# Optimization experiments

Hardware: AMD Instinct MI355X
Metric: run time of the kernel (lower is better)

The kernel has to match this reference:

```python
import jax, jax.numpy as jnp
import numpy as np
import math

N_NODES, N_EDGES = 10000, 160000
CS, CZ, CH, NH, PQ, PV = 384, 128, 192, 12, 4, 8
INF, EPS = 100000.0, 1e-8


def setup_inputs() -> dict:
    key = jax.random.key(0)
    ks = iter(jax.random.split(key, 48))

    def rn(shape, scale=1.0):
        return jax.random.normal(next(ks), shape, jnp.float32) * scale

    def lin(din, dout):
        return rn((din, dout), 1.0 / math.sqrt(din)), jnp.zeros((dout,), jnp.float32)

    s = rn((N_NODES, CS))
    z = rn((N_EDGES, CZ))
    edge_index = jax.random.randint(next(ks), (2, N_EDGES), 0, N_NODES)
    # proper random rotations via QR (sign-corrected)
    A = rn((N_NODES, 3, 3))
    Q, R = jnp.linalg.qr(A)
    rots = Q * jnp.sign(jnp.diagonal(R, axis1=-2, axis2=-1))[:, None, :]
    trans = rn((N_NODES, 3), 10.0)
    mask = jnp.ones((N_NODES,), jnp.float32)
    Ww1, bw1 = lin(2 * CS + CZ, CH)
    Ww2, bw2 = lin(CH, CH)
    Ww3, bw3 = lin(CH, NH)
    Wv1, bv1 = lin(CS + CZ, CH)
    Wv2, bv2 = lin(CH, CH)
    Wv3, bv3 = lin(CH, CH)
    Wq, bq = lin(CS, NH * PQ * 3)
    Wkv, bkv = lin(CS, NH * (PQ + PV) * 3)
    Wb, bb = lin(CZ, NH)
    Wdz, bdz = lin(CZ, CZ // 4)
    Wo, bo = lin(NH * (CZ // 4 + CH // NH + PV * 4), CS)
    hw = jnp.full((NH,), math.log(math.e - 1.0), jnp.float32)  # softplus^-1(1)
    return dict(s=s, z=z, edge_index=edge_index, rots=rots, trans=trans, mask=mask,
                Ww1=Ww1, bw1=bw1, Ww2=Ww2, bw2=bw2, Ww3=Ww3, bw3=bw3,
                Wv1=Wv1, bv1=bv1, Wv2=Wv2, bv2=bv2, Wv3=Wv3, bv3=bv3,
                Wq=Wq, bq=bq, Wkv=Wkv, bkv=bkv, Wb=Wb, bb=bb,
                Wdz=Wdz, bdz=bdz, Wo=Wo, bo=bo, hw=hw)


def _points(flat, rots, t, P):
    # flat [N, 3P] is coord-major (split into 3 chunks then stacked last): p[n, p, c] = flat[n, c*P + p]
    p = flat.reshape(flat.shape[0], 3, P).transpose(0, 2, 1)
    return jnp.einsum('nij,npj->npi', rots, p) + t[:, None, :]


def _forward(s, z, edge_index, rots, trans, mask,
             Ww1, bw1, Ww2, bw2, Ww3, bw3,
             Wv1, bv1, Wv2, bv2, Wv3, bv3,
             Wq, bq, Wkv, bkv, Wb, bb, Wdz, bdz, Wo, bo, hw):
    n = s.shape[0]
    src = edge_index[1]
    dst = edge_index[0]
    t = trans * 0.1  # r.scale_translation(1/10)
    q_pts = _points(s @ Wq + bq, rots, t, NH * PQ).reshape(n, NH, PQ, 3)
    kv_pts = _points(s @ Wkv + bkv, rots, t, NH * (PQ + PV)).reshape(n, NH, PQ + PV, 3)
    k_pts, v_pts = kv_pts[:, :, :PQ], kv_pts[:, :, PQ:]
    b = z @ Wb + bb  # [E, NH]
    w_ins = jnp.concatenate([s[src], s[dst], z], axis=-1)  # [E, 2*CS+CZ]
    h = jax.nn.relu(w_ins @ Ww1 + bw1)
    h = jax.nn.relu(h @ Ww2 + bw2)
    a = (h @ Ww3 + bw3) * math.sqrt(1.0 / (3 * CH)) + math.sqrt(1.0 / 3) * b
    disp = q_pts[src] - k_pts[dst]  # [E, NH, PQ, 3]
    pt_att = jnp.sum(disp ** 2, axis=-1)  # [E, NH, PQ]
    hw_sp = jax.nn.softplus(hw)[None, :, None] * math.sqrt(1.0 / (3 * (PQ * 9.0 / 2)))
    pt_att = jnp.sum(pt_att * hw_sp, axis=-1) * (-0.5)  # [E, NH]
    edge_mask = INF * (mask[dst] * mask[src] - 1.0)
    a = a + pt_att + edge_mask[:, None]
    # segment softmax grouped by edge_index[1]
    amax = jax.ops.segment_max(a, src, num_segments=n)
    ex = jnp.exp(a - amax[src])
    denom = jax.ops.segment_sum(ex, src, num_segments=n)
    a = ex / (denom[src] + 1e-16)
    v_in = jnp.concatenate([s[dst], z], axis=-1)
    h = jax.nn.relu(v_in @ Wv1 + bv1)
    h = jax.nn.relu(h @ Wv2 + bv2)
    v_dst = (h @ Wv3 + bv3).reshape(-1, NH, CH // NH)
    o = jax.ops.segment_sum(a[..., None] * v_dst, src, num_segments=n).reshape(n, -1)
    o_pt = jax.ops.segment_sum(a[..., None, None] * v_pts[dst], src, num_segments=n)  # [n, NH, PV, 3]
    o_pt = jnp.einsum('nji,nhpj->nhpi', rots, o_pt - t[:, None, None, :])  # invert_apply: R^T (x - t)
    o_pt_norm = jnp.sqrt(jnp.sum(o_pt ** 2, axis=-1) + EPS).reshape(n, -1)
    o_pt_flat = o_pt.reshape(n, NH * PV, 3)
    pair_z = z @ Wdz + bdz  # [E, CZ//4]
    o_pair = jax.ops.segment_sum(a[..., None] * pair_z[:, None, :], src, num_segments=n).reshape(n, -1)
    feats = jnp.concatenate([o, o_pt_flat[..., 0], o_pt_flat[..., 1], o_pt_flat[..., 2], o_pt_norm, o_pair], axis=-1)
    return feats @ Wo + bo


def reference(s, z, edge_index, rots, trans, mask,
              Ww1, bw1, Ww2, bw2, Ww3, bw3,
              Wv1, bv1, Wv2, bv2, Wv3, bv3,
              Wq, bq, Wkv, bkv, Wb, bb, Wdz, bdz, Wo, bo, hw):
    return _forward(s, z, edge_index, rots, trans, mask,
                    Ww1, bw1, Ww2, bw2, Ww3, bw3,
                    Wv1, bv1, Wv2, bv2, Wv3, bv3,
                    Wq, bq, Wkv, bkv, Wb, bb, Wdz, bdz, Wo, bo, hw)
```

## Files before the change

kernel.cpp:

```cpp
#include <hip/hip_runtime.h>
#include <hip/hip_bf16.h>
#include <math.h>

#define N_NODES 10000
#define N_EDGES 160000
#define CS 384
#define CZ 128
#define CH 192
#define NH 12
#define PQ 4
#define PV 8

typedef __hip_bfloat16 bf16;
typedef unsigned short ushort;
typedef __attribute__((ext_vector_type(8))) short short8;
typedef __attribute__((ext_vector_type(4))) short s16x4;
typedef __attribute__((ext_vector_type(4))) float f32x4;

__device__ __forceinline__ ushort cvt1(float f) {
  bf16 h = __float2bfloat16(f);
  return __builtin_bit_cast(unsigned short, h);
}
__device__ __forceinline__ short8 lda8f(const float* p, int idx) {
  const f32x4* q = (const f32x4*)(p + idx);
  f32x4 a = q[0], b = q[1];
  short8 r;
  r[0] = (short)cvt1(a[0]); r[1] = (short)cvt1(a[1]);
  r[2] = (short)cvt1(a[2]); r[3] = (short)cvt1(a[3]);
  r[4] = (short)cvt1(b[0]); r[5] = (short)cvt1(b[1]);
  r[6] = (short)cvt1(b[2]); r[7] = (short)cvt1(b[3]);
  return r;
}
__device__ __forceinline__ float bf(ushort u) {
  return __bfloat162float(__builtin_bit_cast(bf16, u));
}

#define OFF_QPTS   0
#define OFF_KPTS   (OFF_QPTS + N_NODES*72)
#define OFF_VPTSH  (OFF_KPTS + N_NODES*72)
#define OFF_SB     (OFF_VPTSH + N_NODES*144)
#define OFF_LOGIT  (OFF_SB + N_NODES*192)
#define OFF_AMAX   (OFF_LOGIT + N_EDGES*12)
#define OFF_DENOM  (OFF_AMAX + N_NODES*12)
#define OFF_ACCO   (OFF_DENOM + N_NODES*12)
#define OFF_ACCP   (OFF_ACCO + N_NODES*192)
#define OFF_ACCZ   (OFF_ACCP + N_NODES*288)
#define FP32_TOTAL (OFF_ACCZ + N_NODES*384)

#define WW1S 0
#define WW2S 172032
#define WW3S 208896
#define WBS  211968
#define WV1S 214016
#define WV2S 312320
#define WV3S 349184
#define WDZS 386048
#define WQS  390144
#define WKVS 445440
#define WOS  611328
#define SWZ_TOTAL 979968

#define IHIST   0
#define ICUR    10000
#define IROWPTR 20000
#define IPERM   30016

__global__ void k_init(float* __restrict__ ws, int* __restrict__ ib) {
  int idx = blockIdx.x * blockDim.x + threadIdx.x;
  const int ntot = N_NODES * (192 + 288 + 384);
  if (idx < ntot) ws[OFF_ACCO + idx] = 0.0f;
  if (idx < N_NODES) ib[IHIST + idx] = 0;
}

__global__ void k_cast_s(const float* __restrict__ s, ushort* __restrict__ sb) {
  int i = (blockIdx.x * 256 + threadIdx.x) * 4;
  if (i + 3 < N_NODES*CS) {
    f32x4 v = *(const f32x4*)(s + i);
    sb[i]   = cvt1(v[0]); sb[i+1] = cvt1(v[1]);
    sb[i+2] = cvt1(v[2]); sb[i+3] = cvt1(v[3]);
  }
}

struct SwzArgs {
  const float* src[11];
  int off[11], start[11], Nreal[11], NT[11];
};
__global__ void k_swz_all(SwzArgs A, ushort* __restrict__ dst, int grand) {
  int tid = blockIdx.x * blockDim.x + threadIdx.x;
  if (tid >= grand) return;
  int m = 0;
  while (m < 10 && tid >= A.start[m+1]) ++m;
  int t = tid - A.start[m];
  int j = t & 7, lane = (t >> 3) & 63, t2 = t >> 9;
  int nt = t2 % A.NT[m], kt = t2 / A.NT[m];
  int k = kt*32 + (lane >> 4)*8 + j;
  int n = nt*16 + (lane & 15);
  dst[A.off[m] + t] = (n < A.Nreal[m]) ? cvt1(A.src[m][k*A.Nreal[m] + n]) : (ushort)0;
}

__global__ void k_hist(const int* __restrict__ ei, int* __restrict__ ib) {
  int e = blockIdx.x * 256 + threadIdx.x;
  if (e < N_EDGES) atomicAdd(&ib[IHIST + ei[N_EDGES + e]], 1);
}

__global__ __launch_bounds__(1024) void k_scan(int* __restrict__ ib) {
  __shared__ int csum[1024];
  int t = threadIdx.x;
  const int CHUNK = (N_NODES + 1023) / 1024;
  int beg = t * CHUNK;
  int end = beg + CHUNK; if (end > N_NODES) end = N_NODES;
  int s = 0;
  for (int i = beg; i < end && i < N_NODES; ++i) s += ib[IHIST + i];
  csum[t] = s;
  __syncthreads();
  for (int off = 1; off < 1024; off <<= 1) {
    int v = (t >= off) ? csum[t - off] : 0;
    __syncthreads();
    csum[t] += v;
    __syncthreads();
  }
  int run = (t == 0) ? 0 : csum[t - 1];
  for (int i = beg; i < end && i < N_NODES; ++i) {
    ib[IROWPTR + i] = run;
    ib[ICUR + i] = run;
    run += ib[IHIST + i];
  }
  if (t == 1023) ib[IROWPTR + N_NODES] = run;
}

__global__ void k_scatter(const int* __restrict__ ei, int* __restrict__ ib) {
  int e = blockIdx.x * 256 + threadIdx.x;
  if (e < N_EDGES) {
    int pos = atomicAdd(&ib[ICUR + ei[N_EDGES + e]], 1);
    ib[IPERM + pos] = e;
  }
}

__global__ __launch_bounds__(256) void k_node_proj_mfma(
    const ushort* __restrict__ sb, const float* __restrict__ rots, const float* __restrict__ trans,
    const ushort* __restrict__ wswz,
    const float* __restrict__ bq, const float* __restrict__ bkv,
    float* __restrict__ ws) {
  const int n0 = blockIdx.x * 32;
  const int tid = threadIdx.x;
  const int wave = tid >> 6, lane = tid & 63, quad = lane >> 4, l16 = lane & 15;
  const int rowhalf = wave & 1, thalf = wave >> 1;
  __shared__ __align__(16) bf16 pbuf[32][584];
  __shared__ float RmL[32][9], tvL[32][3];
  for (int i = tid; i < 32*9; i += 256) {
    int nl = i/9, j = i - nl*9; int nd = n0 + nl;
    RmL[nl][j] = (nd < N_NODES) ? rots[nd*9 + j] : 0.f;
  }
  for (int i = tid; i < 32*3; i += 256) {
    int nl = i/3, j = i - nl*3; int nd = n0 + nl;
    tvL[nl][j] = (nd < N_NODES) ? 0.1f * trans[nd*3 + j] : 0.f;
  }

  const int row = rowhalf*16 + l16;
  int nd = n0 + row;
  const int nclamp = (nd < N_NODES) ? nd : 0;
  f32x4 acc[18];
#pragma unroll
  for (int i = 0; i < 18; ++i) acc[i] = (f32x4){0.f, 0.f, 0.f, 0.f};
  const short8* bq8 = (const short8*)(wswz + WQS);
  const short8* bkv8 = (const short8*)(wswz + WKVS);
#pragma unroll 2
  for (int kt = 0; kt < 12; ++kt) {
    short8 av = *(const short8*)(sb + nclamp*384 + kt*32 + quad*8);
#pragma unroll
    for (int nt = 0; nt < 18; ++nt) {
      int g = thalf*18 + nt;
      short8 bv = (g < 9) ? bq8[(kt*9 + g)*64 + lane]
                          : bkv8[(kt*27 + (g - 9))*64 + lane];
      acc[nt] = __builtin_amdgcn_mfma_f32_16x16x32_bf16(av, bv, acc[nt], 0, 0, 0);
    }
  }
#pragma unroll
  for (int nt = 0; nt < 18; ++nt) {
    int gcol = (thalf*18 + nt)*16 + l16;
    float bias = (gcol < 144) ? bq[gcol] : bkv[gcol - 144];
#pragma unroll
    for (int r = 0; r < 4; ++r)
      pbuf[rowhalf*16 + quad*4 + r][gcol] = __float2bfloat16(acc[nt][r] + bias);
  }
  __syncthreads();

  bf16* qpb = (bf16*)(ws + OFF_QPTS);
  bf16* kpb = (bf16*)(ws + OFF_KPTS);
  bf16* vph = (bf16*)(ws + OFF_VPTSH);
  for (int i = tid; i < 32*192; i += 256) {
    int nl = i / 192, p = i - nl*192;
    int node = n0 + nl;
    if (node >= N_NODES) continue;
    float c0, c1, c2;
    if (p < 48) {
      c0 = __bfloat162float(pbuf[nl][p]);
      c1 = __bfloat162float(pbuf[nl][48 + p]);
      c2 = __bfloat162float(pbuf[nl][96 + p]);
    } else {
      int q = p - 48;
      c0 = __bfloat162float(pbuf[nl][144 + q]);
      c1 = __bfloat162float(pbuf[nl][288 + q]);
      c2 = __bfloat162float(pbuf[nl][432 + q]);
    }
    const float* Rm = RmL[nl];
    const float* tv = tvL[nl];
    float r0 = Rm[0]*c0 + Rm[1]*c1 + Rm[2]*c2 + tv[0];
    float r1 = Rm[3]*c0 + Rm[4]*c1 + Rm[5]*c2 + tv[1];
    float r2 = Rm[6]*c0 + Rm[7]*c1 + Rm[8]*c2 + tv[2];
    if (p < 48) {
      int base = node*144 + p*3;
      qpb[base]   = __float2bfloat16(r0);
      qpb[base+1] = __float2bfloat16(r1);
      qpb[base+2] = __float2bfloat16(r2);
    } else {
      int q = p - 48; int h = q / 12, idx = q % 12;
      if (idx < PQ) {
        int base = node*144 + (h*PQ + idx)*3;
        kpb[base]   = __float2bfloat16(r0);
        kpb[base+1] = __float2bfloat16(r1);
        kpb[base+2] = __float2bfloat16(r2);
      } else {
        int base = node*288 + (h*PV + (idx - PQ))*3;
        vph[base]   = __float2bfloat16(r0);
        vph[base+1] = __float2bfloat16(r1);
        vph[base+2] = __float2bfloat16(r2);
      }
    }
  }
}

__global__ __launch_bounds__(256) void k_edge_logit_mfma(
    const ushort* __restrict__ sb, const float* __restrict__ zp, const int* __restrict__ ei,
    const float* __restrict__ mask,
    const ushort* __restrict__ wswz,
    const float* __restrict__ bw1, const float* __restrict__ bw2, const float* __restrict__ bw3,
    const float* __restrict__ bb, const float* __restrict__ hw,
    const ushort* __restrict__ qpb, const ushort* __restrict__ kpb,
    const int* __restrict__ ib,
    float* __restrict__ logit) {
  const int e0 = blockIdx.x * 64;
  const int tid = threadIdx.x;
  const int wave = tid >> 6, lane = tid & 63, quad = lane >> 4, l16 = lane & 15;
  __shared__ __align__(16) bf16 hbuf[64][200];
  __shared__ int seL[64], deL[64], eIdL[64];
  if (tid < 64) {
    int e = ib[IPERM + e0 + tid];
    eIdL[tid] = e; deL[tid] = ei[e]; seL[tid] = ei[N_EDGES + e];
  }
  __syncthreads();

  const int r0 = wave*16 + l16;
  const int es0 = seL[r0], ed0 = deL[r0], ez0 = eIdL[r0];

  f32x4 acc0[12];
#pragma unroll
  for (int i = 0; i < 12; ++i) acc0[i] = (f32x4){0.f, 0.f, 0.f, 0.f};
  f32x4 accB0 = (f32x4){0.f, 0.f, 0.f, 0.f};
  const short8* bw = (const short8*)(wswz + WW1S);
  const short8* bB8 = (const short8*)(wswz + WBS);
#pragma unroll 2
  for (int kt = 0; kt < 12; ++kt) {
    int k0 = kt*32 + quad*8;
    short8 a0 = *(const short8*)(sb + es0*384 + k0);
    const short8* bk = bw + (kt*12*64 + lane);
#pragma unroll
    for (int nt = 0; nt < 12; ++nt) {
      short8 bv = bk[nt*64];
      acc0[nt] = __builtin_amdgcn_mfma_f32_16x16x32_bf16(a0, bv, acc0[nt], 0, 0, 0);
    }
  }
#pragma unroll 2
  for (int kt = 12; kt < 24; ++kt) {
    int k0 = (kt - 12)*32 + quad*8;
    short8 a0 = *(const short8*)(sb + ed0*384 + k0);
    const short8* bk = bw + (kt*12*64 + lane);
#pragma unroll
    for (int nt = 0; nt < 12; ++nt) {
      short8 bv = bk[nt*64];
      acc0[nt] = __builtin_amdgcn_mfma_f32_16x16x32_bf16(a0, bv, acc0[nt], 0, 0, 0);
    }
  }
#pragma unroll 2
  for (int kt = 24; kt < 28; ++kt) {
    int k0 = (kt - 24)*32 + quad*8;
    short8 a0 = lda8f(zp, ez0*128 + k0);
    const short8* bk = bw + (kt*12*64 + lane);
#pragma unroll
    for (int nt = 0; nt < 12; ++nt) {
      short8 bv = bk[nt*64];
      acc0[nt] = __builtin_amdgcn_mfma_f32_16x16x32_bf16(a0, bv, acc0[nt], 0, 0, 0);
    }
    short8 bvB = bB8[(kt - 24)*64 + lane];
    accB0 = __builtin_amdgcn_mfma_f32_16x16x32_bf16(a0, bvB, accB0, 0, 0, 0);
  }
#pragma unroll
  for (int nt = 0; nt < 12; ++nt) {
    float bcol = bw1[nt*16 + l16];
#pragma unroll
    for (int r = 0; r < 4; ++r)
      hbuf[wave*16 + quad*4 + r][nt*16 + l16] =
          __float2bfloat16(fmaxf(acc0[nt][r] + bcol, 0.f));
  }

#pragma unroll
  for (int i = 0; i < 12; ++i) acc0[i] = (f32x4){0.f, 0.f, 0.f, 0.f};
  bw = (const short8*)(wswz + WW2S);
#pragma unroll
  for (int kt = 0; kt < 6; ++kt) {
    short8 a0 = *(const short8*)&hbuf[r0][kt*32 + quad*8];
    const short8* bk = bw + (kt*12*64 + lane);
#pragma unroll
    for (int nt = 0; nt < 12; ++nt) {
      short8 bv = bk[nt*64];
      acc0[nt] = __builtin_amdgcn_mfma_f32_16x16x32_bf16(a0, bv, acc0[nt], 0, 0, 0);
    }
  }
#pragma unroll
  for (int nt = 0; nt < 12; ++nt) {
    float bcol = bw2[nt*16 + l16];
#pragma unroll
    for (int r = 0; r < 4; ++r)
      hbuf[wave*16 + quad*4 + r][nt*16 + l16] =
          __float2bfloat16(fmaxf(acc0[nt][r] + bcol, 0.f));
  }

  f32x4 accW0 = (f32x4){0.f, 0.f, 0.f, 0.f};
  const short8* b3 = (const short8*)(wswz + WW3S);
#pragma unroll
  for (int kt = 0; kt < 6; ++kt) {
    short8 a0 = *(const short8*)&hbuf[r0][kt*32 + quad*8];
    short8 bv = b3[kt*64 + lane];
    accW0 = __builtin_amdgcn_mfma_f32_16x16x32_bf16(a0, bv, accW0, 0, 0, 0);
  }

  if (l16 < 12) {
    const int h = l16;
    float hv = hw[h];
    float hws = logf(1.0f + expf(hv)) * 0.1360827634879543f;
    float b3c = bw3[h], bbc = bb[h];
#pragma unroll
    for (int r = 0; r < 4; ++r) {
      int eloc = wave*16 + quad*4 + r;
      int se = seL[eloc], de = deL[eloc];
      float v = (accW0[r] + b3c) * 0.041666666666666664f + 0.5773502691896258f * (accB0[r] + bbc);
      int qb = se*144 + h*12;
      int kb = de*144 + h*12;
      float pa = 0.f;
#pragma unroll
      for (int t3 = 0; t3 < 3; ++t3) {
        s16x4 qv = *(const s16x4*)(qpb + qb + t3*4);
        s16x4 kv = *(const s16x4*)(kpb + kb + t3*4);
#pragma unroll
        for (int u = 0; u < 4; ++u) {
          float d = bf((ushort)qv[u]) - bf((ushort)kv[u]);
          pa += d*d;
        }
      }
      v -= 0.5f * hws * pa;
      v += 100000.0f * (mask[de] * mask[se] - 1.0f);
      logit[(e0 + eloc)*12 + h] = v;
    }
  }
}

__global__ void k_softmax(float* __restrict__ a, const int* __restrict__ ib) {
  int t = blockIdx.x * 256 + threadIdx.x;
  if (t >= N_NODES * 12) return;
  int n = t / 12, h = t - n*12;
  int b = ib[IROWPTR + n], e = ib[IROWPTR + n + 1];
  if (b == e) return;
  float m = -3.4e38f;
  for (int j = b; j < e; ++j) m = fmaxf(m, a[j*12 + h]);
  float s = 0.f;
  for (int j = b; j < e; ++j) {
    float ex = expf(a[j*12 + h] - m);
    s += ex;
    a[j*12 + h] = ex;
  }
  float inv = 1.f / (s + 1e-16f);
  for (int j = b; j < e; ++j) a[j*12 + h] *= inv;
}

__global__ __launch_bounds__(256) void k_edge_accum_mfma(
    const ushort* __restrict__ sb, const float* __restrict__ zp, const int* __restrict__ ei,
    const ushort* __restrict__ wswz,
    const float* __restrict__ bv1, const float* __restrict__ bv2, const float* __restrict__ bv3,
    const float* __restrict__ bdz,
    const float* __restrict__ aS,
    const bf16* __restrict__ vph, const int* __restrict__ ib,
    float* __restrict__ acc_o, float* __restrict__ acc_p, float* __restrict__ acc_z) {
  const int p0 = blockIdx.x * 64;
  const int tid = threadIdx.x;
  const int wave = tid >> 6, lane = tid & 63, quad = lane >> 4, l16 = lane & 15;
  __shared__ __align__(16) unsigned char smem[64*193*4];
  __shared__ float awL[64][12];
  __shared__ int seL[64], deL[64], eIdL[64];
  bf16* hb = (bf16*)smem;
  float* stg = (float*)smem;
  if (tid < 64) {
    int e = ib[IPERM + p0 + tid];
    eIdL[tid] = e;
    deL[tid] = ei[e];
    seL[tid] = ei[N_EDGES + e];
  }
  __syncthreads();
  for (int i = tid; i < 64*12; i += 256)
    (&awL[0][0])[i] = aS[p0*12 + i];

  const int arow = wave*16 + l16;
  const int edst = deL[arow];
  const int eid  = eIdL[arow];

  f32x4 acc[12];
#pragma unroll
  for (int i = 0; i < 12; ++i) acc[i] = (f32x4){0.f, 0.f, 0.f, 0.f};
  f32x4 apz[2];
  apz[0] = (f32x4){0.f, 0.f, 0.f, 0.f};
  apz[1] = (f32x4){0.f, 0.f, 0.f, 0.f};
  const short8* bw = (const short8*)(wswz + WV1S);
  const short8* bz = (const short8*)(wswz + WDZS);
#pragma unroll 2
  for (int kt = 0; kt < 12; ++kt) {
    short8 av = *(const short8*)(sb + edst*384 + kt*32 + quad*8);
    const short8* bk = bw + (kt*12*64 + lane);
#pragma unroll
    for (int nt = 0; nt < 12; ++nt) {
      short8 bv = bk[nt*64];
      acc[nt] = __builtin_amdgcn_mfma_f32_16x16x32_bf16(av, bv, acc[nt], 0, 0, 0);
    }
  }
#pragma unroll 2
  for (int kt = 12; kt < 16; ++kt) {
    int kz = (kt - 12)*32 + quad*8;
    short8 av = lda8f(zp, eid*128 + kz);
    const short8* bk = bw + (kt*12*64 + lane);
#pragma unroll
    for (int nt = 0; nt < 12; ++nt) {
      short8 bv = bk[nt*64];
      acc[nt] = __builtin_amdgcn_mfma_f32_16x16x32_bf16(av, bv, acc[nt], 0, 0, 0);
    }
#pragma unroll
    for (int nt = 0; nt < 2; ++nt) {
      short8 bvz = bz[((kt - 12)*2 + nt)*64 + lane];
      apz[nt] = __builtin_amdgcn_mfma_f32_16x16x32_bf16(av, bvz, apz[nt], 0, 0, 0);
    }
  }
#pragma unroll
  for (int nt = 0; nt < 12; ++nt) {
    float bcol = bv1[nt*16 + l16];
#pragma unroll
    for (int r = 0; r < 4; ++r)
      hb[(wave*16 + quad*4 + r)*200 + nt*16 + l16] =
          __float2bfloat16(fmaxf(acc[nt][r] + bcol, 0.f));
  }

#pragma unroll
  for (int i = 0; i < 12; ++i) acc[i] = (f32x4){0.f, 0.f, 0.f, 0.f};
  bw = (const short8*)(wswz + WV2S);
#pragma unroll
  for (int kt = 0; kt < 6; ++kt) {
    short8 av = *(const short8*)&hb[(wave*16 + l16)*200 + kt*32 + quad*8];
    const short8* bk = bw + (kt*12*64 + lane);
#pragma unroll
    for (int nt = 0; nt < 12; ++nt) {
      short8 bv = bk[nt*64];
      acc[nt] = __builtin_amdgcn_mfma_f32_16x16x32_bf16(av, bv, acc[nt], 0, 0, 0);
    }
  }
#pragma unroll
  for (int nt = 0; nt < 12; ++nt) {
    float bcol = bv2[nt*16 + l16];
#pragma unroll
    for (int r = 0; r < 4; ++r)
      hb[(wave*16 + quad*4 + r)*200 + nt*16 + l16] =
          __float2bfloat16(fmaxf(acc[nt][r] + bcol, 0.f));
  }

#pragma unroll
  for (int i = 0; i < 12; ++i) acc[i] = (f32x4){0.f, 0.f, 0.f, 0.f};
  bw = (const short8*)(wswz + WV3S);
#pragma unroll
  for (int kt = 0; kt < 6; ++kt) {
    short8 av = *(const short8*)&hb[(wave*16 + l16)*200 + kt*32 + quad*8];
    const short8* bk = bw + (kt*12*64 + lane);
#pragma unroll
    for (int nt = 0; nt < 12; ++nt) {
      short8 bv = bk[nt*64];
      acc[nt] = __builtin_amdgcn_mfma_f32_16x16x32_bf16(av, bv, acc[nt], 0, 0, 0);
    }
  }
  __syncthreads();

#pragma unroll
  for (int nt = 0; nt < 12; ++nt) {
    int col = nt*16 + l16;
    float bcol = bv3[col];
#pragma unroll
    for (int r = 0; r < 4; ++r) {
      int eloc = wave*16 + quad*4 + r;
      stg[eloc*193 + col] = awL[eloc][nt] * (acc[nt][r] + bcol);
    }
  }
  __syncthreads();
  for (int c = tid; c < 192; c += 256) {
    float sum = 0.f;
    for (int r = 0; r < 64; ++r) {
      sum += stg[r*193 + c];
      if (r == 63 || seL[r+1] != seL[r]) {
        atomicAdd(&acc_o[seL[r]*192 + c], sum);
        sum = 0.f;
      }
    }
  }
  __syncthreads();

#pragma unroll
  for (int nt = 0; nt < 2; ++nt) {
    int c = nt*16 + l16;
    float bcol = bdz[c];
#pragma unroll
    for (int r = 0; r < 4; ++r) {
      int eloc = wave*16 + quad*4 + r;
      stg[eloc*33 + c] = apz[nt][r] + bcol;
    }
  }
  __syncthreads();
  for (int p = tid; p < 384; p += 256) {
    int h = p >> 5, c = p & 31;
    float sum = 0.f;
    for (int r = 0; r < 64; ++r) {
      sum += awL[r][h] * stg[r*33 + c];
      if (r == 63 || seL[r+1] != seL[r]) {
        atomicAdd(&acc_z[seL[r]*384 + h*32 + c], sum);
        sum = 0.f;
      }
    }
  }
  __syncthreads();

  for (int ch = 0; ch < 2; ++ch) {
    for (int i = tid; i < 64*144; i += 256) {
      int eloc = i / 144, jj = i - eloc*144;
      int j = ch*144 + jj;
      int h = j / 24;
      stg[eloc*145 + jj] = awL[eloc][h] * __bfloat162float(vph[deL[eloc]*288 + j]);
    }
    __syncthreads();
    for (int c = tid; c < 144; c += 256) {
      float sum = 0.f;
      for (int r = 0; r < 64; ++r) {
        sum += stg[r*145 + c];
        if (r == 63 || seL[r+1] != seL[r]) {
          atomicAdd(&acc_p[seL[r]*288 + ch*144 + c], sum);
          sum = 0.f;
        }
      }
    }
    __syncthreads();
  }
}

__global__ __launch_bounds__(256) void k_node_out_mfma(
    const float* __restrict__ rots, const float* __restrict__ trans,
    const ushort* __restrict__ wswz, const float* __restrict__ bo,
    const float* __restrict__ acc_o, const float* __restrict__ acc_p,
    const float* __restrict__ acc_z, float* __restrict__ out) {
  const int n0 = blockIdx.x * 32;
  const int tid = threadIdx.x;
  const int wave = tid >> 6, lane = tid & 63, quad = lane >> 4, l16 = lane & 15;
  __shared__ __align__(16) bf16 fbuf[32][968];
  __shared__ float RmL[32][9], tvL[32][3];
  for (int i = tid; i < 32*9; i += 256) {
    int nl = i/9, j = i - nl*9; int nd = n0 + nl;
    RmL[nl][j] = (nd < N_NODES) ? rots[nd*9 + j] : 0.f;
  }
  for (int i = tid; i < 32*3; i += 256) {
    int nl = i/3, j = i - nl*3; int nd = n0 + nl;
    tvL[nl][j] = (nd < N_NODES) ? 0.1f * trans[nd*3 + j] : 0.f;
  }
  __syncthreads();
  for (int i = tid; i < 32*192; i += 256) {
    int nl = i/192, c = i - nl*192; int nd = n0 + nl;
    fbuf[nl][c] = __float2bfloat16((nd < N_NODES) ? acc_o[nd*192 + c] : 0.f);
  }
  for (int i = tid; i < 32*96; i += 256) {
    int nl = i/96, pt = i - nl*96; int nd = n0 + nl;
    float r0 = 0.f, r1 = 0.f, r2 = 0.f, nm = 0.f;
    if (nd < N_NODES) {
      const float* Rm = RmL[nl];
      float v0 = acc_p[nd*288 + pt*3 + 0] - tvL[nl][0];
      float v1 = acc_p[nd*288 + pt*3 + 1] - tvL[nl][1];
      float v2 = acc_p[nd*288 + pt*3 + 2] - tvL[nl][2];
      r0 = Rm[0]*v0 + Rm[3]*v1 + Rm[6]*v2;
      r1 = Rm[1]*v0 + Rm[4]*v1 + Rm[7]*v2;
      r2 = Rm[2]*v0 + Rm[5]*v1 + Rm[8]*v2;
      nm = sqrtf(r0*r0 + r1*r1 + r2*r2 + 1e-8f);
    }
    fbuf[nl][192 + pt] = __float2bfloat16(r0);
    fbuf[nl][288 + pt] = __float2bfloat16(r1);
    fbuf[nl][384 + pt] = __float2bfloat16(r2);
    fbuf[nl][480 + pt] = __float2bfloat16(nm);
  }
  for (int i = tid; i < 32*384; i += 256) {
    int nl = i/384, c = i - nl*384; int nd = n0 + nl;
    fbuf[nl][576 + c] = __float2bfloat16((nd < N_NODES) ? acc_z[nd*384 + c] : 0.f);
  }
  __syncthreads();

  const int rowhalf = wave & 1, thalf = wave >> 1;
  f32x4 acc[12];
#pragma unroll
  for (int i = 0; i < 12; ++i) acc[i] = (f32x4){0.f, 0.f, 0.f, 0.f};
  const short8* bwo = (const short8*)(wswz + WOS);
#pragma unroll 2
  for (int kt = 0; kt < 30; ++kt) {
    short8 av = *(const short8*)&fbuf[rowhalf*16 + l16][kt*32 + quad*8];
#pragma unroll
    for (int nt = 0; nt < 12; ++nt) {
      short8 bv = bwo[(kt*24 + thalf*12 + nt)*64 + lane];
      acc[nt] = __builtin_amdgcn_mfma_f32_16x16x32_bf16(av, bv, acc[nt], 0, 0, 0);
    }
  }
#pragma unroll
  for (int nt = 0; nt < 12; ++nt) {
    int col = (thalf*12 + nt)*16 + l16;
    float bias = bo[col];
#pragma unroll
    for (int r = 0; r < 4; ++r) {
      int nd = n0 + rowhalf*16 + quad*4 + r;
      if (nd < N_NODES) out[nd*384 + col] = acc[nt][r] + bias;
    }
  }
}

extern "C" void kernel_launch(void* const* d_in, const int* in_sizes, int n_in,
                              void* d_out, int out_size, void* d_ws, size_t ws_size,
                              hipStream_t stream) {
  const float* s     = (const float*)d_in[0];
  const float* z     = (const float*)d_in[1];
  const int*   ei    = (const int*)d_in[2];
  const float* rots  = (const float*)d_in[3];
  const float* trans = (const float*)d_in[4];
  const float* mask  = (const float*)d_in[5];
  const float* Ww1 = (const float*)d_in[6];  const float* bw1 = (const float*)d_in[7];
  const float* Ww2 = (const float*)d_in[8];  const float* bw2 = (const float*)d_in[9];
  const float* Ww3 = (const float*)d_in[10]; const float* bw3 = (const float*)d_in[11];
  const float* Wv1 = (const float*)d_in[12]; const float* bv1 = (const float*)d_in[13];
  const float* Wv2 = (const float*)d_in[14]; const float* bv2 = (const float*)d_in[15];
  const float* Wv3 = (const float*)d_in[16]; const float* bv3 = (const float*)d_in[17];
  const float* Wq  = (const float*)d_in[18]; const float* bq  = (const float*)d_in[19];
  const float* Wkv = (const float*)d_in[20]; const float* bkv = (const float*)d_in[21];
  const float* Wb  = (const float*)d_in[22]; const float* bb  = (const float*)d_in[23];
  const float* Wdz = (const float*)d_in[24]; const float* bdz = (const float*)d_in[25];
  const float* Wo  = (const float*)d_in[26]; const float* bo  = (const float*)d_in[27];
  const float* hw  = (const float*)d_in[28];
  float* ws = (float*)d_ws;
  ushort* wswz = (ushort*)(ws + FP32_TOTAL);
  int* ib = (int*)(wswz + SWZ_TOTAL);
  float* out = (float*)d_out;
  ushort* sb = (ushort*)(ws + OFF_SB);

  const int ntot = N_NODES * (192 + 288 + 384);
  k_init<<<(ntot + 255)/256, 256, 0, stream>>>(ws, ib);
  k_cast_s<<<(N_NODES*CS/4 + 255)/256, 256, 0, stream>>>(s, sb);

  SwzArgs A;
  const float* srcs[11] = {Ww1, Ww2, Ww3, Wb, Wv1, Wv2, Wv3, Wdz, Wq, Wkv, Wo};
  int offs[11]   = {WW1S, WW2S, WW3S, WBS, WV1S, WV2S, WV3S, WDZS, WQS, WKVS, WOS};
  int Ks[11]     = {896, 192, 192, 128, 512, 192, 192, 128, 384, 384, 960};
  int Nreals[11] = {192, 192, 12, 12, 192, 192, 192, 32, 144, 432, 384};
  int NTs[11]    = {12, 12, 1, 1, 12, 12, 12, 2, 9, 27, 24};
  int cum = 0;
  for (int m = 0; m < 11; ++m) {
    A.src[m] = srcs[m]; A.off[m] = offs[m]; A.start[m] = cum;
    A.Nreal[m] = Nreals[m]; A.NT[m] = NTs[m];
    cum += (Ks[m]/32) * NTs[m] * 512;
  }
  k_swz_all<<<(cum + 255)/256, 256, 0, stream>>>(A, wswz, cum);

  k_hist<<<(N_EDGES + 255)/256, 256, 0, stream>>>(ei, ib);
  k_scan<<<1, 1024, 0, stream>>>(ib);
  k_scatter<<<(N_EDGES + 255)/256, 256, 0, stream>>>(ei, ib);

  k_node_proj_mfma<<<(N_NODES + 31)/32, 256, 0, stream>>>(
      sb, rots, trans, wswz, bq, bkv, ws);

  k_edge_logit_mfma<<<N_EDGES/64, 256, 0, stream>>>(
      sb, z, ei, mask, wswz,
      bw1, bw2, bw3, bb, hw,
      (const ushort*)(ws + OFF_QPTS), (const ushort*)(ws + OFF_KPTS),
      ib, ws + OFF_LOGIT);

  k_softmax<<<(N_NODES*12 + 255)/256, 256, 0, stream>>>(ws + OFF_LOGIT, ib);

  k_edge_accum_mfma<<<N_EDGES/64, 256, 0, stream>>>(
      sb, z, ei, wswz,
      bv1, bv2, bv3, bdz,
      ws + OFF_LOGIT,
      (const bf16*)(ws + OFF_VPTSH), ib,
      ws + OFF_ACCO, ws + OFF_ACCP, ws + OFF_ACCZ);

  k_node_out_mfma<<<(N_NODES + 31)/32, 256, 0, stream>>>(
      rots, trans, wswz, bo,
      ws + OFF_ACCO, ws + OFF_ACCP, ws + OFF_ACCZ, out);
}
```

Measured before the change: 909.3 us.

## Give each wave private LDS staging and segment-reduce per wave without block barriers

The edge-accumulation kernel now gives each of the four waves its own LDS staging region. The hidden-layer buffers and the scatter-reduction staging are indexed per wave, so the block-wide __syncthreads between epilogue phases are removed. Each wave reduces only its own 16 edges before issuing atomics, and the value-point gather now uses 4-wide bf16 loads. Total LDS use drops and barrier stalls go away. In exchange, segments that span wave boundaries produce more atomics, and the code relies on wave-synchronous LDS visibility with no explicit barrier.

```diff
diff --git a/kernel.cpp b/kernel.cpp
--- a/kernel.cpp
+++ b/kernel.cpp
@@ -393,20 +393,20 @@
   const int p0 = blockIdx.x * 64;
   const int tid = threadIdx.x;
   const int wave = tid >> 6, lane = tid & 63, quad = lane >> 4, l16 = lane & 15;
-  __shared__ __align__(16) unsigned char smem[64*193*4];
+  __shared__ __align__(16) unsigned char smem[4][6656];
   __shared__ float awL[64][12];
   __shared__ int seL[64], deL[64], eIdL[64];
-  bf16* hb = (bf16*)smem;
-  float* stg = (float*)smem;
+  bf16* hb = (bf16*)smem[wave];
+  float* stg = (float*)smem[wave];
   if (tid < 64) {
     int e = ib[IPERM + p0 + tid];
     eIdL[tid] = e;
     deL[tid] = ei[e];
     seL[tid] = ei[N_EDGES + e];
   }
-  __syncthreads();
   for (int i = tid; i < 64*12; i += 256)
     (&awL[0][0])[i] = aS[p0*12 + i];
+  __syncthreads();
 
   const int arow = wave*16 + l16;
   const int edst = deL[arow];
@@ -451,7 +451,7 @@
     float bcol = bv1[nt*16 + l16];
 #pragma unroll
     for (int r = 0; r < 4; ++r)
-      hb[(wave*16 + quad*4 + r)*200 + nt*16 + l16] =
+      hb[(quad*4 + r)*200 + nt*16 + l16] =
           __float2bfloat16(fmaxf(acc[nt][r] + bcol, 0.f));
   }
 
@@ -460,7 +460,7 @@
   bw = (const short8*)(wswz + WV2S);
 #pragma unroll
   for (int kt = 0; kt < 6; ++kt) {
-    short8 av = *(const short8*)&hb[(wave*16 + l16)*200 + kt*32 + quad*8];
+    short8 av = *(const short8*)&hb[l16*200 + kt*32 + quad*8];
     const short8* bk = bw + (kt*12*64 + lane);
 #pragma unroll
     for (int nt = 0; nt < 12; ++nt) {
@@ -473,7 +473,7 @@
     float bcol = bv2[nt*16 + l16];
 #pragma unroll
     for (int r = 0; r < 4; ++r)
-      hb[(wave*16 + quad*4 + r)*200 + nt*16 + l16] =
+      hb[(quad*4 + r)*200 + nt*16 + l16] =
           __float2bfloat16(fmaxf(acc[nt][r] + bcol, 0.f));
   }
 
@@ -482,7 +482,7 @@
   bw = (const short8*)(wswz + WV3S);
 #pragma unroll
   for (int kt = 0; kt < 6; ++kt) {
-    short8 av = *(const short8*)&hb[(wave*16 + l16)*200 + kt*32 + quad*8];
+    short8 av = *(const short8*)&hb[l16*200 + kt*32 + quad*8];
     const short8* bk = bw + (kt*12*64 + lane);
 #pragma unroll
     for (int nt = 0; nt < 12; ++nt) {
@@ -490,74 +490,88 @@
       acc[nt] = __builtin_amdgcn_mfma_f32_16x16x32_bf16(av, bv, acc[nt], 0, 0, 0);
     }
   }
-  __syncthreads();
-
-#pragma unroll
-  for (int nt = 0; nt < 12; ++nt) {
-    int col = nt*16 + l16;
-    float bcol = bv3[col];
-#pragma unroll
-    for (int r = 0; r < 4; ++r) {
-      int eloc = wave*16 + quad*4 + r;
-      stg[eloc*193 + col] = awL[eloc][nt] * (acc[nt][r] + bcol);
-    }
-  }
-  __syncthreads();
-  for (int c = tid; c < 192; c += 256) {
-    float sum = 0.f;
-    for (int r = 0; r < 64; ++r) {
-      sum += stg[r*193 + c];
-      if (r == 63 || seL[r+1] != seL[r]) {
-        atomicAdd(&acc_o[seL[r]*192 + c], sum);
-        sum = 0.f;
+
+#pragma unroll
+  for (int half = 0; half < 2; ++half) {
+#pragma unroll
+    for (int nti = 0; nti < 6; ++nti) {
+      int nt = half*6 + nti;
+      int lc = nti*16 + l16;
+      float bcol = bv3[nt*16 + l16];
+#pragma unroll
+      for (int r = 0; r < 4; ++r) {
+        int lr = quad*4 + r;
+        stg[lr*97 + lc] = awL[wave*16 + lr][nt] * (acc[nt][r] + bcol);
       }
     }
-  }
-  __syncthreads();
-
-#pragma unroll
-  for (int nt = 0; nt < 2; ++nt) {
-    int c = nt*16 + l16;
-    float bcol = bdz[c];
-#pragma unroll
-    for (int r = 0; r < 4; ++r) {
-      int eloc = wave*16 + quad*4 + r;
-      stg[eloc*33 + c] = apz[nt][r] + bcol;
-    }
-  }
-  __syncthreads();
-  for (int p = tid; p < 384; p += 256) {
-    int h = p >> 5, c = p & 31;
-    float sum = 0.f;
-    for (int r = 0; r < 64; ++r) {
-      sum += awL[r][h] * stg[r*33 + c];
-      if (r == 63 || seL[r+1] != seL[r]) {
-        atomicAdd(&acc_z[seL[r]*384 + h*32 + c], sum);
-        sum = 0.f;
-      }
-    }
-  }
-  __syncthreads();
-
-  for (int ch = 0; ch < 2; ++ch) {
-    for (int i = tid; i < 64*144; i += 256) {
-      int eloc = i / 144, jj = i - eloc*144;
-      int j = ch*144 + jj;
-      int h = j / 24;
-      stg[eloc*145 + jj] = awL[eloc][h] * __bfloat162float(vph[deL[eloc]*288 + j]);
-    }
-    __syncthreads();
-    for (int c = tid; c < 144; c += 256) {
+    for (int c = lane; c < 96; c += 64) {
       float sum = 0.f;
-      for (int r = 0; r < 64; ++r) {
-        sum += stg[r*145 + c];
-        if (r == 63 || seL[r+1] != seL[r]) {
-          atomicAdd(&acc_p[seL[r]*288 + ch*144 + c], sum);
+#pragma unroll
+      for (int lr = 0; lr < 16; ++lr) {
+        int gr = wave*16 + lr;
+        sum += stg[lr*97 + c];
+        if (lr == 15 || seL[gr+1] != seL[gr]) {
+          atomicAdd(&acc_o[seL[gr]*192 + half*96 + c], sum);
           sum = 0.f;
         }
       }
     }
-    __syncthreads();
+  }
+
+  {
+#pragma unroll
+    for (int nt = 0; nt < 2; ++nt) {
+      int c = nt*16 + l16;
+      float bcol = bdz[c];
+#pragma unroll
+      for (int r = 0; r < 4; ++r) {
+        int lr = quad*4 + r;
+        stg[lr*33 + c] = apz[nt][r] + bcol;
+      }
+    }
+    for (int p = lane; p < 384; p += 64) {
+      int h = p >> 5, c = p & 31;
+      float sum = 0.f;
+#pragma unroll
+      for (int lr = 0; lr < 16; ++lr) {
+        int gr = wave*16 + lr;
+        sum += awL[gr][h] * stg[lr*33 + c];
+        if (lr == 15 || seL[gr+1] != seL[gr]) {
+          atomicAdd(&acc_z[seL[gr]*384 + h*32 + c], sum);
+          sum = 0.f;
+        }
+      }
+    }
+  }
+
+  for (int ch = 0; ch < 4; ++ch) {
+    for (int i = lane; i < 16*18; i += 64) {
+      int lr = i / 18, g4 = i - lr*18;
+      int jj = g4*4;
+      int j = ch*72 + jj;
+      int h = j / 24;
+      int gr = wave*16 + lr;
+      float aw = awL[gr][h];
+      s16x4 vv = *(const s16x4*)(vph + deL[gr]*288 + j);
+      f32x4 o;
+      o[0] = aw * bf((ushort)vv[0]);
+      o[1] = aw * bf((ushort)vv[1]);
+      o[2] = aw * bf((ushort)vv[2]);
+      o[3] = aw * bf((ushort)vv[3]);
+      *(f32x4*)(stg + lr*76 + jj) = o;
+    }
+    for (int c = lane; c < 72; c += 64) {
+      float sum = 0.f;
+#pragma unroll
+      for (int lr = 0; lr < 16; ++lr) {
+        int gr = wave*16 + lr;
+        sum += stg[lr*76 + c];
+        if (lr == 15 || seL[gr+1] != seL[gr]) {
+          atomicAdd(&acc_p[seL[gr]*288 + ch*72 + c], sum);
+          sum = 0.f;
+        }
+      }
+    }
   }
 }
 
```

After: 1.061 ms. 16.7% more time.

## Precompute per-node first-layer projections to factor the edge MLP input

Applied to the files above, without the earlier changes.

The first layer of the edge weight MLP over [s_src, s_dst, z] is split by linearity. The s_src and s_dst parts are computed once per node in a new k_sp kernel and stored as bf16 in the ACCZ scratch region. Each edge then only runs the z part (K=128) through MFMA and adds the two gathered per-node partial sums, removing about 6/7 of the edge first-layer FLOPs. The cost is an extra small kernel, a separate zeroing pass for ACCZ after reuse, gathered bf16 loads in the epilogue, and an extra bf16 rounding of the partial sums.

```diff
diff --git a/kernel.cpp b/kernel.cpp
--- a/kernel.cpp
+++ b/kernel.cpp
@@ -46,6 +46,9 @@
 #define OFF_ACCP   (OFF_ACCO + N_NODES*192)
 #define OFF_ACCZ   (OFF_ACCP + N_NODES*288)
 #define FP32_TOTAL (OFF_ACCZ + N_NODES*384)
+
+#define SP_SRC_US  0
+#define SP_DST_US  (N_NODES*192)
 
 #define WW1S 0
 #define WW2S 172032
@@ -67,9 +70,14 @@
 
 __global__ void k_init(float* __restrict__ ws, int* __restrict__ ib) {
   int idx = blockIdx.x * blockDim.x + threadIdx.x;
-  const int ntot = N_NODES * (192 + 288 + 384);
+  const int ntot = N_NODES * (192 + 288);
   if (idx < ntot) ws[OFF_ACCO + idx] = 0.0f;
   if (idx < N_NODES) ib[IHIST + idx] = 0;
+}
+
+__global__ void k_zero_accz(float* __restrict__ ws) {
+  int idx = blockIdx.x * blockDim.x + threadIdx.x;
+  if (idx < N_NODES*384) ws[OFF_ACCZ + idx] = 0.0f;
 }
 
 __global__ void k_cast_s(const float* __restrict__ s, ushort* __restrict__ sb) {
@@ -133,6 +141,42 @@
   if (e < N_EDGES) {
     int pos = atomicAdd(&ib[ICUR + ei[N_EDGES + e]], 1);
     ib[IPERM + pos] = e;
+  }
+}
+
+__global__ __launch_bounds__(256) void k_sp(
+    const ushort* __restrict__ sb, const ushort* __restrict__ wswz,
+    ushort* __restrict__ sp) {
+  const int n0 = blockIdx.x * 32;
+  const int tid = threadIdx.x;
+  const int wave = tid >> 6, lane = tid & 63, quad = lane >> 4, l16 = lane & 15;
+  const int rowhalf = wave & 1, part = wave >> 1;
+  const int row = rowhalf*16 + l16;
+  int nd = n0 + row;
+  const int nclamp = (nd < N_NODES) ? nd : 0;
+  f32x4 acc[12];
+#pragma unroll
+  for (int i = 0; i < 12; ++i) acc[i] = (f32x4){0.f, 0.f, 0.f, 0.f};
+  const short8* bw = (const short8*)(wswz + WW1S);
+#pragma unroll 2
+  for (int kt = 0; kt < 12; ++kt) {
+    short8 av = *(const short8*)(sb + nclamp*384 + kt*32 + quad*8);
+    const short8* bk = bw + ((part*12 + kt)*12*64 + lane);
+#pragma unroll
+    for (int nt = 0; nt < 12; ++nt) {
+      short8 bv = bk[nt*64];
+      acc[nt] = __builtin_amdgcn_mfma_f32_16x16x32_bf16(av, bv, acc[nt], 0, 0, 0);
+    }
+  }
+  ushort* dst = sp + (part ? SP_DST_US : SP_SRC_US);
+#pragma unroll
+  for (int nt = 0; nt < 12; ++nt) {
+    int col = nt*16 + l16;
+#pragma unroll
+    for (int r = 0; r < 4; ++r) {
+      int node = n0 + rowhalf*16 + quad*4 + r;
+      if (node < N_NODES) dst[node*192 + col] = cvt1(acc[nt][r]);
+    }
   }
 }
 
@@ -237,6 +281,7 @@
     const float* __restrict__ bw1, const float* __restrict__ bw2, const float* __restrict__ bw3,
     const float* __restrict__ bb, const float* __restrict__ hw,
     const ushort* __restrict__ qpb, const ushort* __restrict__ kpb,
+    const ushort* __restrict__ sps, const ushort* __restrict__ spd,
     const int* __restrict__ ib,
     float* __restrict__ logit) {
   const int e0 = blockIdx.x * 64;
@@ -251,7 +296,7 @@
   __syncthreads();
 
   const int r0 = wave*16 + l16;
-  const int es0 = seL[r0], ed0 = deL[r0], ez0 = eIdL[r0];
+  const int ez0 = eIdL[r0];
 
   f32x4 acc0[12];
 #pragma unroll
@@ -260,47 +305,30 @@
   const short8* bw = (const short8*)(wswz + WW1S);
   const short8* bB8 = (const short8*)(wswz + WBS);
 #pragma unroll 2
-  for (int kt = 0; kt < 12; ++kt) {
+  for (int kt = 0; kt < 4; ++kt) {
     int k0 = kt*32 + quad*8;
-    short8 a0 = *(const short8*)(sb + es0*384 + k0);
-    const short8* bk = bw + (kt*12*64 + lane);
+    short8 a0 = lda8f(zp, ez0*128 + k0);
+    const short8* bk = bw + ((24 + kt)*12*64 + lane);
 #pragma unroll
     for (int nt = 0; nt < 12; ++nt) {
       short8 bv = bk[nt*64];
       acc0[nt] = __builtin_amdgcn_mfma_f32_16x16x32_bf16(a0, bv, acc0[nt], 0, 0, 0);
     }
-  }
-#pragma unroll 2
-  for (int kt = 12; kt < 24; ++kt) {
-    int k0 = (kt - 12)*32 + quad*8;
-    short8 a0 = *(const short8*)(sb + ed0*384 + k0);
-    const short8* bk = bw + (kt*12*64 + lane);
-#pragma unroll
-    for (int nt = 0; nt < 12; ++nt) {
-      short8 bv = bk[nt*64];
-      acc0[nt] = __builtin_amdgcn_mfma_f32_16x16x32_bf16(a0, bv, acc0[nt], 0, 0, 0);
-    }
-  }
-#pragma unroll 2
-  for (int kt = 24; kt < 28; ++kt) {
-    int k0 = (kt - 24)*32 + quad*8;
-    short8 a0 = lda8f(zp, ez0*128 + k0);
-    const short8* bk = bw + (kt*12*64 + lane);
-#pragma unroll
-    for (int nt = 0; nt < 12; ++nt) {
-      short8 bv = bk[nt*64];
-      acc0[nt] = __builtin_amdgcn_mfma_f32_16x16x32_bf16(a0, bv, acc0[nt], 0, 0, 0);
-    }
-    short8 bvB = bB8[(kt - 24)*64 + lane];
+    short8 bvB = bB8[kt*64 + lane];
     accB0 = __builtin_amdgcn_mfma_f32_16x16x32_bf16(a0, bvB, accB0, 0, 0, 0);
   }
 #pragma unroll
   for (int nt = 0; nt < 12; ++nt) {
-    float bcol = bw1[nt*16 + l16];
-#pragma unroll
-    for (int r = 0; r < 4; ++r)
-      hbuf[wave*16 + quad*4 + r][nt*16 + l16] =
-          __float2bfloat16(fmaxf(acc0[nt][r] + bcol, 0.f));
+    int col = nt*16 + l16;
+    float bcol = bw1[col];
+#pragma unroll
+    for (int r = 0; r < 4; ++r) {
+      int row = wave*16 + quad*4 + r;
+      float v = acc0[nt][r] + bcol
+              + bf(sps[seL[row]*192 + col])
+              + bf(spd[deL[row]*192 + col]);
+      hbuf[row][col] = __float2bfloat16(fmaxf(v, 0.f));
+    }
   }
 
 #pragma unroll
@@ -660,8 +688,9 @@
   int* ib = (int*)(wswz + SWZ_TOTAL);
   float* out = (float*)d_out;
   ushort* sb = (ushort*)(ws + OFF_SB);
-
-  const int ntot = N_NODES * (192 + 288 + 384);
+  ushort* sp = (ushort*)(ws + OFF_ACCZ);
+
+  const int ntot = N_NODES * (192 + 288);
   k_init<<<(ntot + 255)/256, 256, 0, stream>>>(ws, ib);
   k_cast_s<<<(N_NODES*CS/4 + 255)/256, 256, 0, stream>>>(s, sb);
 
@@ -686,11 +715,16 @@
   k_node_proj_mfma<<<(N_NODES + 31)/32, 256, 0, stream>>>(
       sb, rots, trans, wswz, bq, bkv, ws);
 
+  k_sp<<<(N_NODES + 31)/32, 256, 0, stream>>>(sb, wswz, sp);
+
   k_edge_logit_mfma<<<N_EDGES/64, 256, 0, stream>>>(
       sb, z, ei, mask, wswz,
       bw1, bw2, bw3, bb, hw,
       (const ushort*)(ws + OFF_QPTS), (const ushort*)(ws + OFF_KPTS),
+      sp + SP_SRC_US, sp + SP_DST_US,
       ib, ws + OFF_LOGIT);
+
+  k_zero_accz<<<(N_NODES*384 + 255)/256, 256, 0, stream>>>(ws);
 
   k_softmax<<<(N_NODES*12 + 255)/256, 256, 0, stream>>>(ws + OFF_LOGIT, ib);
 
```

New measurement: 785.0 us. 13.7% less time.
